# Optimization experiments

Measured on AMD Instinct MI355X. Metric: run time of the kernel, lower is better.

Reference implementation:

```python
import jax, jax.numpy as jnp
import numpy as np

NUM_HEADS = 16
NUM_HIDDENS = 1024
D_K = NUM_HIDDENS // NUM_HEADS
NEG_INF = -1.0e9


def setup_inputs() -> dict:
    key = jax.random.key(0)
    kx, kq, kk, kv, ko, kl = jax.random.split(key, 6)
    B, S, D = 2, 2048, NUM_HIDDENS
    scale = 1.0 / np.sqrt(D)
    return {
        "X": jax.random.normal(kx, (B, S, D), dtype=jnp.float32),
        "valid_lens": jax.random.randint(kl, (B,), 0, S, dtype=jnp.int64),
        "W_q": jax.random.normal(kq, (D, D), dtype=jnp.float32) * scale,
        "W_k": jax.random.normal(kk, (D, D), dtype=jnp.float32) * scale,
        "W_v": jax.random.normal(kv, (D, D), dtype=jnp.float32) * scale,
        "W_o": jax.random.normal(ko, (D, D), dtype=jnp.float32) * scale,
    }


def _split_heads(x):
    # [B, S, D] -> [B, H, S, d_k]
    B, S, _ = x.shape
    return x.reshape(B, S, NUM_HEADS, D_K).transpose(0, 2, 1, 3)


def reference(X, valid_lens, W_q, W_k, W_v, W_o):
    B, S, D = X.shape
    # nn.Linear(bias=False): y = x @ W.T  (W is [out, in])
    Q = _split_heads(jnp.einsum("bsd,ed->bse", X, W_q))  # [B,H,S,dk]
    K = _split_heads(jnp.einsum("bsd,ed->bse", X, W_k))
    V = _split_heads(jnp.einsum("bsd,ed->bse", X, W_v))

    scores = jnp.einsum("bhqd,bhkd->bhqk", Q, K) / jnp.sqrt(
        jnp.asarray(D_K, dtype=X.dtype)
    )  # [B,H,S,S]

    # key-position mask per batch: positions >= valid_len get -1e9
    mask = jnp.arange(S)[None, :] >= valid_lens[:, None]  # [B,S]
    scores = jnp.where(mask[:, None, None, :], jnp.asarray(NEG_INF, X.dtype), scores)

    attn = jax.nn.softmax(scores, axis=-1)  # dropout p=0 -> identity
    out = jnp.einsum("bhqk,bhkd->bhqd", attn, V)  # [B,H,S,dk]
    out = out.transpose(0, 2, 1, 3).reshape(B, S, D)
    return jnp.einsum("bsd,ed->bse", out, W_o)
```

## Files before the change

kernel.cpp:

```cpp
#include <hip/hip_runtime.h>
#include <stdint.h>

#define S_LEN 2048
#define BATCH 2
#define DMODEL 1024
#define NHEAD 16
#define DK 64
#define MROWS (BATCH * S_LEN)

typedef __attribute__((ext_vector_type(8))) short bf16x8;
typedef __attribute__((ext_vector_type(4))) float f32x4;
typedef __attribute__((ext_vector_type(4))) short short4v;
typedef __attribute__((ext_vector_type(2))) uint32_t u32x2;

__device__ __forceinline__ short f2b(float f) {
    union { float f; uint32_t u; } c; c.f = f;
    uint32_t u = c.u;
    return (short)((u + 0x7fffu + ((u >> 16) & 1u)) >> 16);
}

__device__ __forceinline__ void gload16(const void* g, void* l) {
    __builtin_amdgcn_global_load_lds(
        (const __attribute__((address_space(1))) void*)g,
        (__attribute__((address_space(3))) void*)l, 16, 0, 0);
}

__global__ void cvt_kernel(const float* __restrict__ X, const float* __restrict__ Wq,
                           const float* __restrict__ Wk, const float* __restrict__ Wv,
                           const float* __restrict__ Wo,
                           short* __restrict__ Xb, short* __restrict__ Wqb,
                           short* __restrict__ Wkb, short* __restrict__ Wvb,
                           short* __restrict__ Wob) {
    const float* src; short* dst; int n4;
    switch (blockIdx.y) {
        case 0:  src = X;  dst = Xb;  n4 = MROWS * DMODEL / 4;  break;
        case 1:  src = Wq; dst = Wqb; n4 = DMODEL * DMODEL / 4; break;
        case 2:  src = Wk; dst = Wkb; n4 = DMODEL * DMODEL / 4; break;
        case 3:  src = Wv; dst = Wvb; n4 = DMODEL * DMODEL / 4; break;
        default: src = Wo; dst = Wob; n4 = DMODEL * DMODEL / 4; break;
    }
    for (int i = blockIdx.x * blockDim.x + threadIdx.x; i < n4;
         i += gridDim.x * blockDim.x) {
        float4 v = ((const float4*)src)[i];
        short4v o;
        o[0] = f2b(v.x); o[1] = f2b(v.y); o[2] = f2b(v.z); o[3] = f2b(v.w);
        ((short4v*)dst)[i] = o;
    }
}

template <int OUT_F32>
__global__ __launch_bounds__(256) void gemm_bt(
    const short* __restrict__ A,
    const short* __restrict__ Bt0, const short* __restrict__ Bt1,
    const short* __restrict__ Bt2,
    short* __restrict__ Cb0, short* __restrict__ Cb1, short* __restrict__ Cb2,
    float* __restrict__ Cf, int M, int N, int K) {
    __shared__ short sA[128 * 32];
    __shared__ short sB[128 * 32];

    const short* Bt = Bt0;
    short* Cb = Cb0;
    if (blockIdx.z == 1) { Bt = Bt1; Cb = Cb1; }
    else if (blockIdx.z == 2) { Bt = Bt2; Cb = Cb2; }

    const int tid = threadIdx.x;
    const int lane = tid & 63;
    const int wid = tid >> 6;
    const int wr = wid >> 1, wc = wid & 1;
    const int brow = blockIdx.y * 128;
    const int bcol = blockIdx.x * 128;
    const int lr = lane & 15;
    const int kh = (lane >> 4) << 3;
    const int swg = ((lr >> 1) & 3) << 3;
    const int khs = kh ^ swg;

    f32x4 acc[4][4] = {};

    const int idx0 = tid, idx1 = tid + 256;
    const int ar0 = idx0 >> 2, ak0 = ((idx0 & 3) << 3) ^ (((ar0 >> 1) & 3) << 3);
    const int ar1 = idx1 >> 2, ak1 = ((idx1 & 3) << 3) ^ (((ar1 >> 1) & 3) << 3);

    const int nk = K >> 5;
    for (int kt = 0; kt < nk; ++kt) {
        __syncthreads();
        const int k0 = kt << 5;
        gload16(A + (size_t)(brow + ar0) * K + k0 + ak0, &sA[idx0 * 8]);
        gload16(A + (size_t)(brow + ar1) * K + k0 + ak1, &sA[idx1 * 8]);
        gload16(Bt + (size_t)(bcol + ar0) * K + k0 + ak0, &sB[idx0 * 8]);
        gload16(Bt + (size_t)(bcol + ar1) * K + k0 + ak1, &sB[idx1 * 8]);
        __syncthreads();

        bf16x8 a[4], b[4];
#pragma unroll
        for (int mt = 0; mt < 4; ++mt)
            a[mt] = *(const bf16x8*)&sA[(wr * 64 + mt * 16 + lr) * 32 + khs];
#pragma unroll
        for (int nt = 0; nt < 4; ++nt)
            b[nt] = *(const bf16x8*)&sB[(wc * 64 + nt * 16 + lr) * 32 + khs];
#pragma unroll
        for (int mt = 0; mt < 4; ++mt)
#pragma unroll
            for (int nt = 0; nt < 4; ++nt)
                acc[mt][nt] = __builtin_amdgcn_mfma_f32_16x16x32_bf16(
                    a[mt], b[nt], acc[mt][nt], 0, 0, 0);
    }

    const int rbase = (lane >> 4) << 2;
    const bool vtrans = (!OUT_F32) && (blockIdx.z == 2);
#pragma unroll
    for (int mt = 0; mt < 4; ++mt) {
#pragma unroll
        for (int nt = 0; nt < 4; ++nt) {
            if (vtrans) {
                int row0 = brow + wr * 64 + mt * 16 + rbase;
                int col = bcol + wc * 64 + nt * 16 + lr;
                int bb = row0 >> 11, key = row0 & 2047;
                int hh = col >> 6, d = col & 63;
                short4v pk;
#pragma unroll
                for (int j = 0; j < 4; ++j) pk[j] = f2b(acc[mt][nt][j]);
                *(short4v*)&Cb[((size_t)((bb * 16 + hh) * 64 + d)) * S_LEN + key] = pk;
            } else {
#pragma unroll
                for (int j = 0; j < 4; ++j) {
                    int row = brow + wr * 64 + mt * 16 + rbase + j;
                    int col = bcol + wc * 64 + nt * 16 + lr;
                    if (OUT_F32)
                        Cf[(size_t)row * N + col] = acc[mt][nt][j];
                    else
                        Cb[(size_t)row * N + col] = f2b(acc[mt][nt][j]);
                }
            }
        }
    }
}

__global__ __launch_bounds__(256) void attn_kernel(
    const short* __restrict__ Q, const short* __restrict__ K,
    const short* __restrict__ Vt, short* __restrict__ O,
    const int* __restrict__ vlens) {
    __shared__ short sK[2][64 * 64];
    __shared__ short sV[2][64 * 64];
    __shared__ short sP[4][2][16 * 64];

    const int tid = threadIdx.x;
    const int lane = tid & 63;
    const int w = tid >> 6;
    const int id = blockIdx.x;
    const int id2 = ((id & 7) << 6) | (id >> 3);
    const int qb = id2 & 15;
    const int bhx = id2 >> 4;
    const int b = bhx & 1, h = bhx >> 1;
    const int lr = lane & 15;
    const int kh = (lane >> 4) << 3;
    const int rbase = (lane >> 4) << 2;
    const int swq = (lr & 7) << 3;

    int vl = vlens[b];
    if (vl < 0) vl = 0;
    if (vl > S_LEN) vl = S_LEN;
    const bool allm = (vl == 0);
    if (allm) vl = S_LEN;
    const int nT = (vl + 63) >> 6;
    const int nFull = ((vl & 63) == 0) ? nT : nT - 1;

    const size_t rowbase = (size_t)(b * S_LEN) * DMODEL + h * DK;
    const short* vt = Vt + ((size_t)((b * 16 + h) * 64)) * S_LEN;

    const short* qrowA = Q + rowbase + (size_t)(qb * 128 + w * 32 + lr) * DMODEL;
    const short* qrowB = qrowA + 16 * DMODEL;
    bf16x8 qf0a = *(const bf16x8*)(qrowA + kh);
    bf16x8 qf1a = *(const bf16x8*)(qrowA + 32 + kh);
    bf16x8 qf0b = *(const bf16x8*)(qrowB + kh);
    bf16x8 qf1b = *(const bf16x8*)(qrowB + 32 + kh);
    if (allm) {
#pragma unroll
        for (int i = 0; i < 8; ++i) { qf0a[i] = 0; qf1a[i] = 0; qf0b[i] = 0; qf1b[i] = 0; }
    }

    f32x4 oacA[4] = {}, oacB[4] = {};
    float mA = -1e30f, mcA = -1e30f, lA = 0.f;
    float mB = -1e30f, mcB = -1e30f, lB = 0.f;
    const float CEXP = 0.18033688011112042f;
    const float THRADD = 44.361419556f;

    const int lofs0 = lr * 64 + (kh ^ swq);
    const int lofs1 = lr * 64 + ((32 + kh) ^ swq);

    const int kr0 = tid >> 3;
    const int kr1 = kr0 + 32;
    const int kc0 = (((tid & 7) ^ (kr0 & 7)) << 3);
    const int kc1 = (((tid & 7) ^ (kr1 & 7)) << 3);

    const short* kA = K + rowbase + (size_t)kr0 * DMODEL + kc0;
    const short* kB = K + rowbase + (size_t)kr1 * DMODEL + kc1;
    const short* vA = vt + (size_t)kr0 * S_LEN + kc0;
    const short* vB = vt + (size_t)kr1 * S_LEN + kc1;

    gload16(kA, &sK[0][tid * 8]);
    gload16(kB, &sK[0][(tid + 256) * 8]);
    gload16(vA, &sV[0][tid * 8]);
    gload16(vB, &sV[0][(tid + 256) * 8]);
    __syncthreads();

#define SOFTMAX_FRAG(SACC, MRUN, MC, LRUN, OAC, SPW)                            \
    do {                                                                        \
        float t0 = fmaxf(fmaxf(SACC[0][0], SACC[0][1]), SACC[0][2]);            \
        float t1 = fmaxf(fmaxf(SACC[0][3], SACC[1][0]), SACC[1][1]);            \
        float t2 = fmaxf(fmaxf(SACC[1][2], SACC[1][3]), SACC[2][0]);            \
        float t3 = fmaxf(fmaxf(SACC[2][1], SACC[2][2]), SACC[2][3]);            \
        float t4 = fmaxf(fmaxf(SACC[3][0], SACC[3][1]), SACC[3][2]);            \
        float pmax = fmaxf(fmaxf(fmaxf(t0, t1), t2),                            \
                           fmaxf(fmaxf(t3, t4), SACC[3][3]));                   \
        if (__any(pmax > MRUN + THRADD)) {                                      \
            float mx = pmax;                                                    \
            mx = fmaxf(mx, __shfl_xor(mx, 16));                                 \
            mx = fmaxf(mx, __shfl_xor(mx, 32));                                 \
            float scl = __builtin_exp2f((MRUN - mx) * CEXP);                    \
            MRUN = mx;                                                          \
            MC = mx * CEXP;                                                     \
            LRUN *= scl;                                                        \
            _Pragma("unroll")                                                   \
            for (int dt = 0; dt < 4; ++dt)                                      \
                _Pragma("unroll")                                               \
                for (int j = 0; j < 4; ++j) OAC[dt][j] *= scl;                  \
        }                                                                       \
        float p[16];                                                            \
        _Pragma("unroll")                                                       \
        for (int nt = 0; nt < 4; ++nt)                                          \
            _Pragma("unroll")                                                   \
            for (int j = 0; j < 4; ++j)                                         \
                p[nt * 4 + j] = __builtin_exp2f(                                \
                    __builtin_fmaf(SACC[nt][j], CEXP, -MC));                    \
        float ls = ((p[0] + p[1]) + (p[2] + p[3])) +                            \
                   ((p[4] + p[5]) + (p[6] + p[7]));                             \
        ls += ((p[8] + p[9]) + (p[10] + p[11])) +                               \
              ((p[12] + p[13]) + (p[14] + p[15]));                              \
        LRUN += ls;                                                             \
        _Pragma("unroll")                                                       \
        for (int nt = 0; nt < 4; ++nt) {                                        \
            u32x2 r;                                                            \
            asm("v_cvt_pk_bf16_f32 %0, %1, %2"                                  \
                : "=v"(r[0]) : "v"(p[nt * 4 + 0]), "v"(p[nt * 4 + 1]));         \
            asm("v_cvt_pk_bf16_f32 %0, %1, %2"                                  \
                : "=v"(r[1]) : "v"(p[nt * 4 + 2]), "v"(p[nt * 4 + 3]));         \
            *(u32x2*)&SPW[lr * 64 + ((nt * 16 + rbase) ^ swq)] = r;             \
        }                                                                       \
    } while (0)

#define TILE_BODY(MASKED_C)                                                     \
    do {                                                                        \
        constexpr bool MASKED = MASKED_C;                                       \
        const short* sKc = sK[cur];                                             \
        const short* sVc = sV[cur];                                             \
        const short* kL0 = sKc + lofs0;                                         \
        const short* kL1 = sKc + lofs1;                                         \
        f32x4 saccA[4] = {}, saccB[4] = {};                                     \
        __builtin_amdgcn_s_setprio(1);                                          \
        _Pragma("unroll")                                                       \
        for (int nt = 0; nt < 4; ++nt) {                                        \
            bf16x8 kb0 = *(const bf16x8*)&kL0[nt * 1024];                       \
            bf16x8 kb1 = *(const bf16x8*)&kL1[nt * 1024];                       \
            saccA[nt] = __builtin_amdgcn_mfma_f32_16x16x32_bf16(                \
                kb0, qf0a, saccA[nt], 0, 0, 0);                                 \
            saccB[nt] = __builtin_amdgcn_mfma_f32_16x16x32_bf16(                \
                kb0, qf0b, saccB[nt], 0, 0, 0);                                 \
            saccA[nt] = __builtin_amdgcn_mfma_f32_16x16x32_bf16(                \
                kb1, qf1a, saccA[nt], 0, 0, 0);                                 \
            saccB[nt] = __builtin_amdgcn_mfma_f32_16x16x32_bf16(                \
                kb1, qf1b, saccB[nt], 0, 0, 0);                                 \
        }                                                                       \
        __builtin_amdgcn_s_setprio(0);                                          \
        if (MASKED) {                                                           \
            _Pragma("unroll")                                                   \
            for (int nt = 0; nt < 4; ++nt)                                      \
                _Pragma("unroll")                                               \
                for (int j = 0; j < 4; ++j) {                                   \
                    int keyi = t * 64 + nt * 16 + rbase + j;                    \
                    if (keyi >= vl) { saccA[nt][j] = -3.0e38f;                  \
                                      saccB[nt][j] = -3.0e38f; }                \
                }                                                               \
        }                                                                       \
        SOFTMAX_FRAG(saccA, mA, mcA, lA, oacA, (&sP[w][0][0]));                 \
        SOFTMAX_FRAG(saccB, mB, mcB, lB, oacB, (&sP[w][1][0]));                 \
        const short* vL0 = sVc + lofs0;                                         \
        const short* vL1 = sVc + lofs1;                                         \
        __builtin_amdgcn_s_setprio(1);                                          \
        {                                                                       \
            bf16x8 pfA = *(const bf16x8*)&sP[w][0][lofs0];                      \
            bf16x8 pfB = *(const bf16x8*)&sP[w][1][lofs0];                      \
            _Pragma("unroll")                                                   \
            for (int dt = 0; dt < 4; ++dt) {                                    \
                bf16x8 vf = *(const bf16x8*)&vL0[dt * 1024];                    \
                oacA[dt] = __builtin_amdgcn_mfma_f32_16x16x32_bf16(             \
                    vf, pfA, oacA[dt], 0, 0, 0);                                \
                oacB[dt] = __builtin_amdgcn_mfma_f32_16x16x32_bf16(             \
                    vf, pfB, oacB[dt], 0, 0, 0);                                \
            }                                                                   \
            pfA = *(const bf16x8*)&sP[w][0][lofs1];                             \
            pfB = *(const bf16x8*)&sP[w][1][lofs1];                             \
            _Pragma("unroll")                                                   \
            for (int dt = 0; dt < 4; ++dt) {                                    \
                bf16x8 vf = *(const bf16x8*)&vL1[dt * 1024];                    \
                oacA[dt] = __builtin_amdgcn_mfma_f32_16x16x32_bf16(             \
                    vf, pfA, oacA[dt], 0, 0, 0);                                \
                oacB[dt] = __builtin_amdgcn_mfma_f32_16x16x32_bf16(             \
                    vf, pfB, oacB[dt], 0, 0, 0);                                \
            }                                                                   \
        }                                                                       \
        __builtin_amdgcn_s_setprio(0);                                          \
    } while (0)

    int cur = 0;
    for (int t = 0; t < nT; ++t) {
        const bool hn = (t + 1 < nT);
        if (hn) {
            short* sKn = sK[cur ^ 1];
            short* sVn = sV[cur ^ 1];
            kA += 64 * DMODEL; kB += 64 * DMODEL;
            vA += 64; vB += 64;
            gload16(kA, &sKn[tid * 8]);
            gload16(kB, &sKn[(tid + 256) * 8]);
            gload16(vA, &sVn[tid * 8]);
            gload16(vB, &sVn[(tid + 256) * 8]);
        }

        if (t < nFull) TILE_BODY(false);
        else TILE_BODY(true);

        __syncthreads();
        cur ^= 1;
    }
#undef TILE_BODY
#undef SOFTMAX_FRAG

    float ltA = lA + __shfl_xor(lA, 16);
    ltA += __shfl_xor(ltA, 32);
    float rlA = 1.f / ltA;
    float ltB = lB + __shfl_xor(lB, 16);
    ltB += __shfl_xor(ltB, 32);
    float rlB = 1.f / ltB;

    short* orowA = O + rowbase + (size_t)(qb * 128 + w * 32 + lr) * DMODEL;
    short* orowB = orowA + 16 * DMODEL;
#pragma unroll
    for (int dt = 0; dt < 4; ++dt) {
        short4v pkA, pkB;
#pragma unroll
        for (int j = 0; j < 4; ++j) {
            pkA[j] = f2b(oacA[dt][j] * rlA);
            pkB[j] = f2b(oacB[dt][j] * rlB);
        }
        *(short4v*)&orowA[dt * 16 + rbase] = pkA;
        *(short4v*)&orowB[dt * 16 + rbase] = pkB;
    }
}

extern "C" void kernel_launch(void* const* d_in, const int* in_sizes, int n_in,
                              void* d_out, int out_size, void* d_ws, size_t ws_size,
                              hipStream_t stream) {
    const float* X = (const float*)d_in[0];
    const int* vlens = (const int*)d_in[1];
    const float* Wq = (const float*)d_in[2];
    const float* Wk = (const float*)d_in[3];
    const float* Wv = (const float*)d_in[4];
    const float* Wo = (const float*)d_in[5];
    float* out = (float*)d_out;

    short* Xb = (short*)d_ws;
    short* Wqb = Xb + (size_t)MROWS * DMODEL;
    short* Wkb = Wqb + (size_t)DMODEL * DMODEL;
    short* Wvb = Wkb + (size_t)DMODEL * DMODEL;
    short* Wob = Wvb + (size_t)DMODEL * DMODEL;
    short* Qb = Wob + (size_t)DMODEL * DMODEL;
    short* Kb = Qb + (size_t)MROWS * DMODEL;
    short* Vtb = Kb + (size_t)MROWS * DMODEL;
    short* Ob = Vtb + (size_t)MROWS * DMODEL;

    cvt_kernel<<<dim3(512, 5), 256, 0, stream>>>(X, Wq, Wk, Wv, Wo, Xb, Wqb, Wkb,
                                                 Wvb, Wob);
    gemm_bt<0><<<dim3(8, 32, 3), 256, 0, stream>>>(Xb, Wqb, Wkb, Wvb, Qb, Kb, Vtb,
                                                   nullptr, MROWS, DMODEL, DMODEL);
    attn_kernel<<<dim3(512), 256, 0, stream>>>(Qb, Kb, Vtb, Ob, vlens);
    gemm_bt<1><<<dim3(8, 32, 1), 256, 0, stream>>>(Ob, Wob, Wob, Wob, nullptr,
                                                   nullptr, nullptr, out, MROWS,
                                                   DMODEL, DMODEL);
}
```

Baseline: 116.6 us.

## Double-buffer LDS tiles in projection GEMM to overlap loads with MFMA

The GEMM now keeps two LDS buffers for the A and B tiles and issues the global-to-LDS loads for the next k-tile before computing on the current one. This cuts one barrier per iteration and is meant to hide global load latency behind the MFMA work. It also raises wave priority around the MFMA block with s_setprio. LDS use per block doubles, which may lower occupancy. The asynchronous LDS loads must also have completed by the single barrier, which depends on the compiler inserting vmcnt waits.

```diff
diff --git a/kernel.cpp b/kernel.cpp
--- a/kernel.cpp
+++ b/kernel.cpp
@@ -55,8 +55,8 @@
     const short* __restrict__ Bt2,
     short* __restrict__ Cb0, short* __restrict__ Cb1, short* __restrict__ Cb2,
     float* __restrict__ Cf, int M, int N, int K) {
-    __shared__ short sA[128 * 32];
-    __shared__ short sB[128 * 32];
+    __shared__ short sA[2][128 * 32];
+    __shared__ short sB[2][128 * 32];
 
     const short* Bt = Bt0;
     short* Cb = Cb0;
@@ -80,29 +80,46 @@
     const int ar0 = idx0 >> 2, ak0 = ((idx0 & 3) << 3) ^ (((ar0 >> 1) & 3) << 3);
     const int ar1 = idx1 >> 2, ak1 = ((idx1 & 3) << 3) ^ (((ar1 >> 1) & 3) << 3);
 
+    const short* gA0 = A + (size_t)(brow + ar0) * K + ak0;
+    const short* gA1 = A + (size_t)(brow + ar1) * K + ak1;
+    const short* gB0 = Bt + (size_t)(bcol + ar0) * K + ak0;
+    const short* gB1 = Bt + (size_t)(bcol + ar1) * K + ak1;
+
     const int nk = K >> 5;
+    gload16(gA0, &sA[0][idx0 * 8]);
+    gload16(gA1, &sA[0][idx1 * 8]);
+    gload16(gB0, &sB[0][idx0 * 8]);
+    gload16(gB1, &sB[0][idx1 * 8]);
+    __syncthreads();
+
+    int cur = 0;
     for (int kt = 0; kt < nk; ++kt) {
-        __syncthreads();
-        const int k0 = kt << 5;
-        gload16(A + (size_t)(brow + ar0) * K + k0 + ak0, &sA[idx0 * 8]);
-        gload16(A + (size_t)(brow + ar1) * K + k0 + ak1, &sA[idx1 * 8]);
-        gload16(Bt + (size_t)(bcol + ar0) * K + k0 + ak0, &sB[idx0 * 8]);
-        gload16(Bt + (size_t)(bcol + ar1) * K + k0 + ak1, &sB[idx1 * 8]);
-        __syncthreads();
+        if (kt + 1 < nk) {
+            const int k0 = (kt + 1) << 5;
+            gload16(gA0 + k0, &sA[cur ^ 1][idx0 * 8]);
+            gload16(gA1 + k0, &sA[cur ^ 1][idx1 * 8]);
+            gload16(gB0 + k0, &sB[cur ^ 1][idx0 * 8]);
+            gload16(gB1 + k0, &sB[cur ^ 1][idx1 * 8]);
+        }
 
         bf16x8 a[4], b[4];
 #pragma unroll
         for (int mt = 0; mt < 4; ++mt)
-            a[mt] = *(const bf16x8*)&sA[(wr * 64 + mt * 16 + lr) * 32 + khs];
+            a[mt] = *(const bf16x8*)&sA[cur][(wr * 64 + mt * 16 + lr) * 32 + khs];
 #pragma unroll
         for (int nt = 0; nt < 4; ++nt)
-            b[nt] = *(const bf16x8*)&sB[(wc * 64 + nt * 16 + lr) * 32 + khs];
+            b[nt] = *(const bf16x8*)&sB[cur][(wc * 64 + nt * 16 + lr) * 32 + khs];
+        __builtin_amdgcn_s_setprio(1);
 #pragma unroll
         for (int mt = 0; mt < 4; ++mt)
 #pragma unroll
             for (int nt = 0; nt < 4; ++nt)
                 acc[mt][nt] = __builtin_amdgcn_mfma_f32_16x16x32_bf16(
                     a[mt], b[nt], acc[mt][nt], 0, 0, 0);
+        __builtin_amdgcn_s_setprio(0);
+
+        __syncthreads();
+        cur ^= 1;
     }
 
     const int rbase = (lane >> 4) << 2;
```

Result: faster. 107.1 us (-8.1%).

## Triple-buffer LDS tiles with vmcnt-based waits in GEMM and attention

Applied to the files above, without the earlier changes.

Both the projection GEMM and the attention kernel now keep three LDS stages and issue global-to-LDS loads two tiles ahead. Each iteration waits with an explicit s_waitcnt vmcnt plus a single barrier, replacing the two __syncthreads per iteration and the single-buffer GEMM. The GEMM MFMA loop also gets a raised wave priority. Attention blocks are remapped so the heads of a given XCD share K/V across batch and query tiles. The cost is more LDS per block, which may lower occupancy, and correctness now depends on hand-counted vmcnt values.

```diff
diff --git a/kernel.cpp b/kernel.cpp
--- a/kernel.cpp
+++ b/kernel.cpp
@@ -12,6 +12,8 @@
 typedef __attribute__((ext_vector_type(4))) float f32x4;
 typedef __attribute__((ext_vector_type(4))) short short4v;
 typedef __attribute__((ext_vector_type(2))) uint32_t u32x2;
+
+#define VMCNT(N) asm volatile("s_waitcnt vmcnt(" #N ")" ::: "memory")
 
 __device__ __forceinline__ short f2b(float f) {
     union { float f; uint32_t u; } c; c.f = f;
@@ -55,8 +57,8 @@
     const short* __restrict__ Bt2,
     short* __restrict__ Cb0, short* __restrict__ Cb1, short* __restrict__ Cb2,
     float* __restrict__ Cf, int M, int N, int K) {
-    __shared__ short sA[128 * 32];
-    __shared__ short sB[128 * 32];
+    __shared__ short sA[3][128 * 32];
+    __shared__ short sB[3][128 * 32];
 
     const short* Bt = Bt0;
     short* Cb = Cb0;
@@ -80,30 +82,52 @@
     const int ar0 = idx0 >> 2, ak0 = ((idx0 & 3) << 3) ^ (((ar0 >> 1) & 3) << 3);
     const int ar1 = idx1 >> 2, ak1 = ((idx1 & 3) << 3) ^ (((ar1 >> 1) & 3) << 3);
 
+    const short* gA0 = A + (size_t)(brow + ar0) * K + ak0;
+    const short* gA1 = A + (size_t)(brow + ar1) * K + ak1;
+    const short* gB0 = Bt + (size_t)(bcol + ar0) * K + ak0;
+    const short* gB1 = Bt + (size_t)(bcol + ar1) * K + ak1;
+
+#define G_STAGE(KT, PA, PB)                                   \
+    do {                                                      \
+        const int k0_ = (KT) << 5;                            \
+        gload16(gA0 + k0_, (PA) + idx0 * 8);                  \
+        gload16(gA1 + k0_, (PA) + idx1 * 8);                  \
+        gload16(gB0 + k0_, (PB) + idx0 * 8);                  \
+        gload16(gB1 + k0_, (PB) + idx1 * 8);                  \
+    } while (0)
+
     const int nk = K >> 5;
+    short* pA0 = &sA[0][0]; short* pA1 = &sA[1][0]; short* pA2 = &sA[2][0];
+    short* pB0 = &sB[0][0]; short* pB1 = &sB[1][0]; short* pB2 = &sB[2][0];
+
+    G_STAGE(0, pA0, pB0);
+    G_STAGE(1, pA1, pB1);
+
     for (int kt = 0; kt < nk; ++kt) {
-        __syncthreads();
-        const int k0 = kt << 5;
-        gload16(A + (size_t)(brow + ar0) * K + k0 + ak0, &sA[idx0 * 8]);
-        gload16(A + (size_t)(brow + ar1) * K + k0 + ak1, &sA[idx1 * 8]);
-        gload16(Bt + (size_t)(bcol + ar0) * K + k0 + ak0, &sB[idx0 * 8]);
-        gload16(Bt + (size_t)(bcol + ar1) * K + k0 + ak1, &sB[idx1 * 8]);
-        __syncthreads();
+        if (kt == nk - 1) { VMCNT(0); } else { VMCNT(4); }
+        __builtin_amdgcn_s_barrier();
+        if (kt + 2 < nk) G_STAGE(kt + 2, pA2, pB2);
 
         bf16x8 a[4], b[4];
 #pragma unroll
         for (int mt = 0; mt < 4; ++mt)
-            a[mt] = *(const bf16x8*)&sA[(wr * 64 + mt * 16 + lr) * 32 + khs];
+            a[mt] = *(const bf16x8*)&pA0[(wr * 64 + mt * 16 + lr) * 32 + khs];
 #pragma unroll
         for (int nt = 0; nt < 4; ++nt)
-            b[nt] = *(const bf16x8*)&sB[(wc * 64 + nt * 16 + lr) * 32 + khs];
+            b[nt] = *(const bf16x8*)&pB0[(wc * 64 + nt * 16 + lr) * 32 + khs];
+        __builtin_amdgcn_s_setprio(1);
 #pragma unroll
         for (int mt = 0; mt < 4; ++mt)
 #pragma unroll
             for (int nt = 0; nt < 4; ++nt)
                 acc[mt][nt] = __builtin_amdgcn_mfma_f32_16x16x32_bf16(
                     a[mt], b[nt], acc[mt][nt], 0, 0, 0);
-    }
+        __builtin_amdgcn_s_setprio(0);
+
+        short* tA = pA0; pA0 = pA1; pA1 = pA2; pA2 = tA;
+        short* tB = pB0; pB0 = pB1; pB1 = pB2; pB2 = tB;
+    }
+#undef G_STAGE
 
     const int rbase = (lane >> 4) << 2;
     const bool vtrans = (!OUT_F32) && (blockIdx.z == 2);
@@ -139,18 +163,19 @@
     const short* __restrict__ Q, const short* __restrict__ K,
     const short* __restrict__ Vt, short* __restrict__ O,
     const int* __restrict__ vlens) {
-    __shared__ short sK[2][64 * 64];
-    __shared__ short sV[2][64 * 64];
+    __shared__ short sK[3][64 * 64];
+    __shared__ short sV[3][64 * 64];
     __shared__ short sP[4][2][16 * 64];
 
     const int tid = threadIdx.x;
     const int lane = tid & 63;
     const int w = tid >> 6;
     const int id = blockIdx.x;
-    const int id2 = ((id & 7) << 6) | (id >> 3);
-    const int qb = id2 & 15;
-    const int bhx = id2 >> 4;
-    const int b = bhx & 1, h = bhx >> 1;
+    const int xcd = id & 7;
+    const int r = id >> 3;
+    const int b = (r >> 5) & 1;
+    const int h = (xcd << 1) | (r & 1);
+    const int qb = (r >> 1) & 15;
     const int lr = lane & 15;
     const int kh = (lane >> 4) << 3;
     const int rbase = (lane >> 4) << 2;
@@ -187,21 +212,20 @@
     const int lofs0 = lr * 64 + (kh ^ swq);
     const int lofs1 = lr * 64 + ((32 + kh) ^ swq);
 
-    const int kr0 = tid >> 3;
-    const int kr1 = kr0 + 32;
-    const int kc0 = (((tid & 7) ^ (kr0 & 7)) << 3);
-    const int kc1 = (((tid & 7) ^ (kr1 & 7)) << 3);
-
-    const short* kA = K + rowbase + (size_t)kr0 * DMODEL + kc0;
-    const short* kB = K + rowbase + (size_t)kr1 * DMODEL + kc1;
-    const short* vA = vt + (size_t)kr0 * S_LEN + kc0;
-    const short* vB = vt + (size_t)kr1 * S_LEN + kc1;
-
-    gload16(kA, &sK[0][tid * 8]);
-    gload16(kB, &sK[0][(tid + 256) * 8]);
-    gload16(vA, &sV[0][tid * 8]);
-    gload16(vB, &sV[0][(tid + 256) * 8]);
-    __syncthreads();
+    const int kr = tid >> 3;
+    const int kc = (((tid & 7) ^ (kr & 7)) << 3);
+    const short* kBase = K + rowbase + (size_t)kr * DMODEL + kc;
+    const short* vBase = vt + (size_t)kr * S_LEN + kc;
+
+#define A_STAGE(T, PK, PV)                                                      \
+    do {                                                                        \
+        const short* kg_ = kBase + (size_t)((T) * 64) * DMODEL;                 \
+        gload16(kg_, (PK) + tid * 8);                                           \
+        gload16(kg_ + (size_t)32 * DMODEL, (PK) + (tid + 256) * 8);             \
+        const short* vg_ = vBase + (T) * 64;                                    \
+        gload16(vg_, (PV) + tid * 8);                                           \
+        gload16(vg_ + (size_t)32 * S_LEN, (PV) + (tid + 256) * 8);              \
+    } while (0)
 
 #define SOFTMAX_FRAG(SACC, MRUN, MC, LRUN, OAC, SPW)                            \
     do {                                                                        \
@@ -239,22 +263,20 @@
         LRUN += ls;                                                             \
         _Pragma("unroll")                                                       \
         for (int nt = 0; nt < 4; ++nt) {                                        \
-            u32x2 r;                                                            \
+            u32x2 r_;                                                           \
             asm("v_cvt_pk_bf16_f32 %0, %1, %2"                                  \
-                : "=v"(r[0]) : "v"(p[nt * 4 + 0]), "v"(p[nt * 4 + 1]));         \
+                : "=v"(r_[0]) : "v"(p[nt * 4 + 0]), "v"(p[nt * 4 + 1]));        \
             asm("v_cvt_pk_bf16_f32 %0, %1, %2"                                  \
-                : "=v"(r[1]) : "v"(p[nt * 4 + 2]), "v"(p[nt * 4 + 3]));         \
-            *(u32x2*)&SPW[lr * 64 + ((nt * 16 + rbase) ^ swq)] = r;             \
+                : "=v"(r_[1]) : "v"(p[nt * 4 + 2]), "v"(p[nt * 4 + 3]));        \
+            *(u32x2*)&SPW[lr * 64 + ((nt * 16 + rbase) ^ swq)] = r_;            \
         }                                                                       \
     } while (0)
 
-#define TILE_BODY(MASKED_C)                                                     \
+#define TILE_BODY(MASKED_C, PK, PV)                                             \
     do {                                                                        \
         constexpr bool MASKED = MASKED_C;                                       \
-        const short* sKc = sK[cur];                                             \
-        const short* sVc = sV[cur];                                             \
-        const short* kL0 = sKc + lofs0;                                         \
-        const short* kL1 = sKc + lofs1;                                         \
+        const short* kL0 = (PK) + lofs0;                                        \
+        const short* kL1 = (PK) + lofs1;                                        \
         f32x4 saccA[4] = {}, saccB[4] = {};                                     \
         __builtin_amdgcn_s_setprio(1);                                          \
         _Pragma("unroll")                                                       \
@@ -283,8 +305,8 @@
         }                                                                       \
         SOFTMAX_FRAG(saccA, mA, mcA, lA, oacA, (&sP[w][0][0]));                 \
         SOFTMAX_FRAG(saccB, mB, mcB, lB, oacB, (&sP[w][1][0]));                 \
-        const short* vL0 = sVc + lofs0;                                         \
-        const short* vL1 = sVc + lofs1;                                         \
+        const short* vL0 = (PV) + lofs0;                                        \
+        const short* vL1 = (PV) + lofs1;                                        \
         __builtin_amdgcn_s_setprio(1);                                          \
         {                                                                       \
             bf16x8 pfA = *(const bf16x8*)&sP[w][0][lofs0];                      \
@@ -311,28 +333,26 @@
         __builtin_amdgcn_s_setprio(0);                                          \
     } while (0)
 
-    int cur = 0;
+    short* pK0 = &sK[0][0]; short* pK1 = &sK[1][0]; short* pK2 = &sK[2][0];
+    short* pV0 = &sV[0][0]; short* pV1 = &sV[1][0]; short* pV2 = &sV[2][0];
+
+    A_STAGE(0, pK0, pV0);
+    if (nT > 1) A_STAGE(1, pK1, pV1);
+
     for (int t = 0; t < nT; ++t) {
-        const bool hn = (t + 1 < nT);
-        if (hn) {
-            short* sKn = sK[cur ^ 1];
-            short* sVn = sV[cur ^ 1];
-            kA += 64 * DMODEL; kB += 64 * DMODEL;
-            vA += 64; vB += 64;
-            gload16(kA, &sKn[tid * 8]);
-            gload16(kB, &sKn[(tid + 256) * 8]);
-            gload16(vA, &sVn[tid * 8]);
-            gload16(vB, &sVn[(tid + 256) * 8]);
-        }
-
-        if (t < nFull) TILE_BODY(false);
-        else TILE_BODY(true);
-
-        __syncthreads();
-        cur ^= 1;
+        if (t == nT - 1) { VMCNT(0); } else { VMCNT(4); }
+        __builtin_amdgcn_s_barrier();
+        if (t + 2 < nT) A_STAGE(t + 2, pK2, pV2);
+
+        if (t < nFull) TILE_BODY(false, pK0, pV0);
+        else TILE_BODY(true, pK0, pV0);
+
+        short* tK = pK0; pK0 = pK1; pK1 = pK2; pK2 = tK;
+        short* tV = pV0; pV0 = pV1; pV1 = pV2; pV2 = tV;
     }
 #undef TILE_BODY
 #undef SOFTMAX_FRAG
+#undef A_STAGE
 
     float ltA = lA + __shfl_xor(lA, 16);
     ltA += __shfl_xor(ltA, 32);
```

Result: faster. 104.5 us (-10.4%).
